# Kernel tuning notes

Measured on AMD Instinct MI355X. Metric: run time of the kernel, lower is better.

The kernel has to match this reference:

```python
import jax, jax.numpy as jnp
import numpy as np

B, T, N = 32, 24, 512
DIM_IN, DIM_OUT, HID, EMB = 64, 2, 128, 16
NEG_SLOPE = 0.01  # nn.LeakyReLU default


def leaky_relu(x):
    return jnp.where(x >= 0, x, NEG_SLOPE * x)


def setup_inputs() -> dict:
    key = jax.random.key(0)
    ks = jax.random.split(key, 11)
    return {
        "eb": jax.random.normal(ks[0], (B, T, N, DIM_IN), jnp.float32),
        "time_eb": jax.random.normal(ks[1], (B, T, EMB), jnp.float32),
        "node_eb": jax.random.normal(ks[2], (N, EMB), jnp.float32),
        # ln1: Linear(dim_in, hidden) stored as [dim_in, hidden] (x @ W + b)
        "W1": jax.random.normal(ks[3], (DIM_IN, HID), jnp.float32) / np.sqrt(DIM_IN),
        "b1": jax.random.normal(ks[4], (HID,), jnp.float32) * 0.01,
        # ln3: Linear(hidden, dim_out)
        "W3": jax.random.normal(ks[5], (HID, DIM_OUT), jnp.float32) / np.sqrt(HID),
        "b3": jax.random.normal(ks[6], (DIM_OUT,), jnp.float32) * 0.01,
        "weights_pool_spa": jax.random.normal(ks[7], (EMB, HID, HID), jnp.float32),
        "bias_pool_spa": jax.random.normal(ks[8], (EMB, HID), jnp.float32),
        "weights_pool_tem": jax.random.normal(ks[9], (EMB, HID, HID), jnp.float32),
        "bias_pool_tem": jax.random.normal(ks[10], (EMB, HID), jnp.float32),
    }


def reference(eb, time_eb, node_eb, W1, b1, W3, b3,
              weights_pool_spa, bias_pool_spa,
              weights_pool_tem, bias_pool_tem):
    # eb: [b,t,n,dim_in] -> [b,t,n,hidden]
    eb_out = eb @ W1 + b1
    # spatial hypernetwork: per-node weight [n,hid,hid] and bias [n,hid]
    weights_spa = jnp.einsum('nd,dio->nio', node_eb, weights_pool_spa)
    bias_spa = node_eb @ bias_pool_spa  # [n,hid]
    out_spa = leaky_relu(jnp.einsum('btni,nio->btno', eb_out, weights_spa) + bias_spa)
    # temporal hypernetwork: per-(b,t) weight [b,t,hid,hid] and bias [b,t,1,hid]
    weights_tem = jnp.einsum('btd,dio->btio', time_eb, weights_pool_tem)
    bias_tem = (time_eb @ bias_pool_tem)[:, :, None, :]
    out_tem = leaky_relu(jnp.einsum('btni,btio->btno', out_spa, weights_tem) + bias_tem)
    logits = out_tem @ W3 + b3  # [b,t,n,dim_out]
    return logits
```

## Files before the change

kernel.cpp:

```cpp
#include <hip/hip_runtime.h>
#include <hip/hip_bf16.h>
#include <stdint.h>

#define BT   768
#define NN   512
#define DIN  64
#define HID  128
#define EMB  16
#define SLOPE 0.01f

typedef __attribute__((ext_vector_type(8))) short bf16x8;
typedef __attribute__((ext_vector_type(4))) float f32x4;
typedef __attribute__((ext_vector_type(4))) short short4v;

__device__ __forceinline__ short f2bf(float f) {
    uint32_t u = __float_as_uint(f);
    u += 0x7fff + ((u >> 16) & 1);
    return (short)(u >> 16);
}
__device__ __forceinline__ float bf2f(short s) {
    return __uint_as_float(((uint32_t)(unsigned short)s) << 16);
}

static const size_t OFF_WSPA = 0;
static const size_t OFF_WTEM = 16777216;
static const size_t OFF_BSPA = 41943040;
static const size_t OFF_BTEM = 42205184;
static const size_t OFF_PTS  = 42598400;
static const size_t OFF_PTT  = 43122688;
static const size_t OFF_W1T  = 43646976;
static const size_t OFF_H2   = 43663360;

__global__ __launch_bounds__(256)
void k_prep(const float* __restrict__ pool_spa, const float* __restrict__ pool_tem,
            const float* __restrict__ W1, short* __restrict__ pts,
            short* __restrict__ ptt, short* __restrict__ w1t)
{
    const int b = blockIdx.x, t = threadIdx.x;
    if (b == 128) {
        int o = t >> 1, kh = (t & 1) * 32;
        for (int k = 0; k < 32; ++k)
            w1t[o * 64 + kh + k] = f2bf(W1[(kh + k) * HID + o]);
        return;
    }
    const float* pool = (b < 64) ? pool_spa : pool_tem;
    short* outp = (b < 64) ? pts : ptt;
    const int bb = b & 63;
    const int d = bb >> 2, o0 = (bb & 3) * 32;
    __shared__ short s[32 * 136];
    #pragma unroll
    for (int c = 0; c < 16; ++c) {
        int e = c * 256 + t;
        int i = e >> 5, oo = e & 31;
        s[oo * 136 + i] = f2bf(pool[(d * HID + i) * HID + o0 + oo]);
    }
    __syncthreads();
    #pragma unroll
    for (int c = 0; c < 8; ++c) {
        int e = c * 256 + t;
        int oo = e >> 6, ii = (e & 63) * 2;
        uint32_t lo = (unsigned short)s[oo * 136 + ii];
        uint32_t hi = (unsigned short)s[oo * 136 + ii + 1];
        ((uint32_t*)outp)[((d * HID + o0 + oo) * HID + ii) >> 1] = lo | (hi << 16);
    }
}

__global__ __launch_bounds__(256)
void k_genw(const short* __restrict__ pts, const short* __restrict__ ptt,
            const float* __restrict__ node_eb, const float* __restrict__ time_eb,
            short* __restrict__ wspa, short* __restrict__ wtem)
{
    const int t = threadIdx.x;
    const bool spa = blockIdx.y < 8;
    const int nb = spa ? blockIdx.y : blockIdx.y - 8;
    const short* pool = spa ? pts : ptt;
    const float* emb = spa ? node_eb : time_eb;
    short* outp = spa ? wspa : wtem;
    __shared__ float sEmb[64 * EMB];
    #pragma unroll
    for (int c = 0; c < 4; ++c) {
        int idx = c * 256 + t;
        sEmb[idx] = emb[nb * 64 * EMB + idx];
    }
    __syncthreads();
    const int cq = blockIdx.x * 256 + t;
    float4 p[EMB];
    #pragma unroll
    for (int d = 0; d < EMB; ++d) {
        short4v v = ((const short4v*)pool)[d * 4096 + cq];
        p[d] = make_float4(bf2f(v.x), bf2f(v.y), bf2f(v.z), bf2f(v.w));
    }
    for (int nn = 0; nn < 64; ++nn) {
        float4 a = make_float4(0.f, 0.f, 0.f, 0.f);
        #pragma unroll
        for (int d = 0; d < EMB; ++d) {
            float e = sEmb[nn * EMB + d];
            a.x += e * p[d].x; a.y += e * p[d].y;
            a.z += e * p[d].z; a.w += e * p[d].w;
        }
        short4v o;
        o.x = f2bf(a.x); o.y = f2bf(a.y); o.z = f2bf(a.z); o.w = f2bf(a.w);
        ((short4v*)outp)[(size_t)(nb * 64 + nn) * 4096 + cq] = o;
    }
}

__global__ __launch_bounds__(256)
void k_genb(const float* __restrict__ bp_spa, const float* __restrict__ bp_tem,
            const float* __restrict__ node_eb, const float* __restrict__ time_eb,
            float* __restrict__ bspa, float* __restrict__ btem)
{
    int q = blockIdx.x * 256 + threadIdx.x;
    const float *bp, *emb; float* outp;
    if (q < NN * 32) { bp = bp_spa; emb = node_eb; outp = bspa; }
    else { q -= NN * 32; bp = bp_tem; emb = time_eb; outp = btem; }
    const int n = q >> 5, oq = q & 31;
    float4 a = make_float4(0.f, 0.f, 0.f, 0.f);
    #pragma unroll
    for (int d = 0; d < EMB; ++d) {
        float e = emb[n * EMB + d];
        float4 b = ((const float4*)bp)[d * 32 + oq];
        a.x += e * b.x; a.y += e * b.y; a.z += e * b.z; a.w += e * b.w;
    }
    ((float4*)outp)[q] = a;
}

__global__ __launch_bounds__(256)
void k_spatial(const float* __restrict__ eb, const short* __restrict__ w1t,
               const float* __restrict__ b1, const short* __restrict__ wspa,
               const float* __restrict__ bspa, short* __restrict__ h2)
{
    const int n = blockIdx.x, R0 = blockIdx.y * 64;
    const int t = threadIdx.x;
    const int wave = t >> 6, lane = t & 63, quad = lane >> 4, l15 = lane & 15;
    const int m0 = (wave >> 1) * 32, n0 = (wave & 1) * 64;

    __shared__ short sH1[64 * 136];
    __shared__ short sU[128 * 136];
    __shared__ float sB1[128], sBs[128];
    short* sEb = sU;
    short* sW1 = sU + 64 * 72;
    short* sWs = sU;

    #pragma unroll
    for (int c = 0; c < 4; ++c) {
        int idx = c * 256 + t;
        int r = idx >> 4, kq = (idx & 15) * 4;
        float4 v = *(const float4*)(eb + ((size_t)(R0 + r) * NN + n) * DIN + kq);
        short4v s;
        s.x = f2bf(v.x); s.y = f2bf(v.y); s.z = f2bf(v.z); s.w = f2bf(v.w);
        *(short4v*)(sEb + r * 72 + kq) = s;
    }
    #pragma unroll
    for (int c = 0; c < 4; ++c) {
        int idx = c * 256 + t;
        *(bf16x8*)(sW1 + (idx >> 3) * 72 + (idx & 7) * 8) =
            *(const bf16x8*)(w1t + idx * 8);
    }
    if (t < 128) { sB1[t] = b1[t]; sBs[t] = bspa[n * HID + t]; }
    __syncthreads();

    f32x4 acc1[2][4] = {};
    #pragma unroll
    for (int kc = 0; kc < 2; ++kc) {
        bf16x8 a0 = *(const bf16x8*)(sEb + (m0 + l15) * 72 + kc * 32 + quad * 8);
        bf16x8 a1 = *(const bf16x8*)(sEb + (m0 + 16 + l15) * 72 + kc * 32 + quad * 8);
        #pragma unroll
        for (int tc = 0; tc < 4; ++tc) {
            bf16x8 b = *(const bf16x8*)(sW1 + (n0 + tc * 16 + l15) * 72 + kc * 32 + quad * 8);
            acc1[0][tc] = __builtin_amdgcn_mfma_f32_16x16x32_bf16(a0, b, acc1[0][tc], 0, 0, 0);
            acc1[1][tc] = __builtin_amdgcn_mfma_f32_16x16x32_bf16(a1, b, acc1[1][tc], 0, 0, 0);
        }
    }
    #pragma unroll
    for (int tr = 0; tr < 2; ++tr)
        #pragma unroll
        for (int tc = 0; tc < 4; ++tc) {
            int col = n0 + tc * 16 + l15;
            float bb = sB1[col];
            #pragma unroll
            for (int r = 0; r < 4; ++r)
                sH1[(m0 + tr * 16 + quad * 4 + r) * 136 + col] = f2bf(acc1[tr][tc][r] + bb);
        }
    __syncthreads();

    {
        const bf16x8* src = (const bf16x8*)(wspa + (size_t)n * 16384);
        #pragma unroll
        for (int c = 0; c < 8; ++c) {
            int idx = c * 256 + t;
            *(bf16x8*)(sWs + (idx >> 4) * 136 + (idx & 15) * 8) = src[idx];
        }
    }
    __syncthreads();

    f32x4 acc2[2][4] = {};
    #pragma unroll
    for (int kc = 0; kc < 4; ++kc) {
        bf16x8 a0 = *(const bf16x8*)(sH1 + (m0 + l15) * 136 + kc * 32 + quad * 8);
        bf16x8 a1 = *(const bf16x8*)(sH1 + (m0 + 16 + l15) * 136 + kc * 32 + quad * 8);
        #pragma unroll
        for (int tc = 0; tc < 4; ++tc) {
            bf16x8 b = *(const bf16x8*)(sWs + (n0 + tc * 16 + l15) * 136 + kc * 32 + quad * 8);
            acc2[0][tc] = __builtin_amdgcn_mfma_f32_16x16x32_bf16(a0, b, acc2[0][tc], 0, 0, 0);
            acc2[1][tc] = __builtin_amdgcn_mfma_f32_16x16x32_bf16(a1, b, acc2[1][tc], 0, 0, 0);
        }
    }
    __syncthreads();
    #pragma unroll
    for (int tr = 0; tr < 2; ++tr)
        #pragma unroll
        for (int tc = 0; tc < 4; ++tc) {
            int col = n0 + tc * 16 + l15;
            float bb = sBs[col];
            #pragma unroll
            for (int r = 0; r < 4; ++r) {
                float v = acc2[tr][tc][r] + bb;
                v = (v >= 0.f) ? v : SLOPE * v;
                sH1[(m0 + tr * 16 + quad * 4 + r) * 136 + col] = f2bf(v);
            }
        }
    __syncthreads();
    #pragma unroll
    for (int c = 0; c < 4; ++c) {
        int idx = c * 256 + t;
        int row = idx >> 4, col = (idx & 15) * 8;
        *(bf16x8*)(h2 + ((size_t)(R0 + row) * NN + n) * HID + col) =
            *(const bf16x8*)(sH1 + row * 136 + col);
    }
}

__global__ __launch_bounds__(256)
void k_temporal(const short* __restrict__ h2, const short* __restrict__ wtem,
                const float* __restrict__ btem, const float* __restrict__ W3,
                const float* __restrict__ b3, float* __restrict__ out)
{
    const int R = blockIdx.x, t = threadIdx.x;
    const int wave = t >> 6, lane = t & 63, quad = lane >> 4, l15 = lane & 15;
    const int m0 = wave * 16;

    __shared__ short sWt[128 * 136];
    __shared__ short sH2[64 * 136];
    __shared__ float sBt[128], sW3[256];

    {
        const bf16x8* src = (const bf16x8*)(wtem + (size_t)R * 16384);
        #pragma unroll
        for (int c = 0; c < 8; ++c) {
            int idx = c * 256 + t;
            *(bf16x8*)(sWt + (idx >> 4) * 136 + (idx & 15) * 8) = src[idx];
        }
    }
    if (t < 128) sBt[t] = btem[R * HID + t];
    sW3[t] = W3[t];
    const float b30 = b3[0], b31 = b3[1];

    for (int nt = 0; nt < 8; ++nt) {
        __syncthreads();
        const bf16x8* src = (const bf16x8*)(h2 + ((size_t)R * NN + nt * 64) * HID);
        #pragma unroll
        for (int c = 0; c < 4; ++c) {
            int idx = c * 256 + t;
            *(bf16x8*)(sH2 + (idx >> 4) * 136 + (idx & 15) * 8) = src[idx];
        }
        __syncthreads();

        f32x4 acc[8] = {};
        #pragma unroll
        for (int kc = 0; kc < 4; ++kc) {
            bf16x8 a = *(const bf16x8*)(sH2 + (m0 + l15) * 136 + kc * 32 + quad * 8);
            #pragma unroll
            for (int tc = 0; tc < 8; ++tc) {
                bf16x8 b = *(const bf16x8*)(sWt + (tc * 16 + l15) * 136 + kc * 32 + quad * 8);
                acc[tc] = __builtin_amdgcn_mfma_f32_16x16x32_bf16(a, b, acc[tc], 0, 0, 0);
            }
        }
        float pl[4][2] = {};
        #pragma unroll
        for (int tc = 0; tc < 8; ++tc) {
            int o = tc * 16 + l15;
            float bt = sBt[o], w0 = sW3[2 * o], w1 = sW3[2 * o + 1];
            #pragma unroll
            for (int r = 0; r < 4; ++r) {
                float v = acc[tc][r] + bt;
                v = (v >= 0.f) ? v : SLOPE * v;
                pl[r][0] += v * w0;
                pl[r][1] += v * w1;
            }
        }
        #pragma unroll
        for (int m = 1; m <= 8; m <<= 1)
            #pragma unroll
            for (int r = 0; r < 4; ++r) {
                pl[r][0] += __shfl_xor(pl[r][0], m);
                pl[r][1] += __shfl_xor(pl[r][1], m);
            }
        if (l15 == 0) {
            #pragma unroll
            for (int r = 0; r < 4; ++r) {
                int nrow = nt * 64 + m0 + quad * 4 + r;
                *(float2*)(out + ((size_t)R * NN + nrow) * 2) =
                    make_float2(pl[r][0] + b30, pl[r][1] + b31);
            }
        }
    }
}

extern "C" void kernel_launch(void* const* d_in, const int* in_sizes, int n_in,
                              void* d_out, int out_size, void* d_ws, size_t ws_size,
                              hipStream_t stream) {
    const float* eb        = (const float*)d_in[0];
    const float* time_eb   = (const float*)d_in[1];
    const float* node_eb   = (const float*)d_in[2];
    const float* W1        = (const float*)d_in[3];
    const float* b1        = (const float*)d_in[4];
    const float* W3        = (const float*)d_in[5];
    const float* b3        = (const float*)d_in[6];
    const float* pool_spa  = (const float*)d_in[7];
    const float* bpool_spa = (const float*)d_in[8];
    const float* pool_tem  = (const float*)d_in[9];
    const float* bpool_tem = (const float*)d_in[10];
    float* out = (float*)d_out;

    char* ws = (char*)d_ws;
    short* wspa = (short*)(ws + OFF_WSPA);
    short* wtem = (short*)(ws + OFF_WTEM);
    float* bspa = (float*)(ws + OFF_BSPA);
    float* btem = (float*)(ws + OFF_BTEM);
    short* pts  = (short*)(ws + OFF_PTS);
    short* ptt  = (short*)(ws + OFF_PTT);
    short* w1t  = (short*)(ws + OFF_W1T);
    short* h2   = (short*)(ws + OFF_H2);

    k_prep<<<129, 256, 0, stream>>>(pool_spa, pool_tem, W1, pts, ptt, w1t);
    k_genw<<<dim3(16, 20), 256, 0, stream>>>(pts, ptt, node_eb, time_eb, wspa, wtem);
    k_genb<<<160, 256, 0, stream>>>(bpool_spa, bpool_tem, node_eb, time_eb, bspa, btem);
    k_spatial<<<dim3(NN, 12), 256, 0, stream>>>(eb, w1t, b1, wspa, bspa, h2);
    k_temporal<<<BT, 256, 0, stream>>>(h2, wtem, btem, W3, b3, out);
}
```

Before: 248.3 us.

## Fuse bias generation into prep, register-prefetch loads, split temporal kernel over nodes

Folds the k_genb bias-generation work into k_prep as extra blocks, removing one kernel launch. k_spatial now issues all of its global loads (eb, W1, per-node weights, biases) up front into registers so their latency overlaps, and keeps the biases in registers instead of shared memory. k_temporal is split into two blocks per (b,t) over the node dimension, which doubles the grid, and it prefetches the next h2 tile into registers while the current tile is computed. The cost is higher register pressure and the per-(b,t) temporal weight tile now being loaded twice.

```diff
diff --git a/kernel.cpp b/kernel.cpp
--- a/kernel.cpp
+++ b/kernel.cpp
@@ -33,10 +33,30 @@
 
 __global__ __launch_bounds__(256)
 void k_prep(const float* __restrict__ pool_spa, const float* __restrict__ pool_tem,
-            const float* __restrict__ W1, short* __restrict__ pts,
-            short* __restrict__ ptt, short* __restrict__ w1t)
+            const float* __restrict__ W1,
+            const float* __restrict__ bp_spa, const float* __restrict__ bp_tem,
+            const float* __restrict__ node_eb, const float* __restrict__ time_eb,
+            short* __restrict__ pts, short* __restrict__ ptt,
+            short* __restrict__ w1t, float* __restrict__ bspa,
+            float* __restrict__ btem)
 {
     const int b = blockIdx.x, t = threadIdx.x;
+    if (b >= 129) {
+        int q = (b - 129) * 256 + t;
+        const float *bp, *emb; float* outp;
+        if (q < NN * 32) { bp = bp_spa; emb = node_eb; outp = bspa; }
+        else { q -= NN * 32; bp = bp_tem; emb = time_eb; outp = btem; }
+        const int n = q >> 5, oq = q & 31;
+        float4 a = make_float4(0.f, 0.f, 0.f, 0.f);
+        #pragma unroll
+        for (int d = 0; d < EMB; ++d) {
+            float e = emb[n * EMB + d];
+            float4 bv = ((const float4*)bp)[d * 32 + oq];
+            a.x += e * bv.x; a.y += e * bv.y; a.z += e * bv.z; a.w += e * bv.w;
+        }
+        ((float4*)outp)[q] = a;
+        return;
+    }
     if (b == 128) {
         int o = t >> 1, kh = (t & 1) * 32;
         for (int k = 0; k < 32; ++k)
@@ -105,26 +125,6 @@
 }
 
 __global__ __launch_bounds__(256)
-void k_genb(const float* __restrict__ bp_spa, const float* __restrict__ bp_tem,
-            const float* __restrict__ node_eb, const float* __restrict__ time_eb,
-            float* __restrict__ bspa, float* __restrict__ btem)
-{
-    int q = blockIdx.x * 256 + threadIdx.x;
-    const float *bp, *emb; float* outp;
-    if (q < NN * 32) { bp = bp_spa; emb = node_eb; outp = bspa; }
-    else { q -= NN * 32; bp = bp_tem; emb = time_eb; outp = btem; }
-    const int n = q >> 5, oq = q & 31;
-    float4 a = make_float4(0.f, 0.f, 0.f, 0.f);
-    #pragma unroll
-    for (int d = 0; d < EMB; ++d) {
-        float e = emb[n * EMB + d];
-        float4 b = ((const float4*)bp)[d * 32 + oq];
-        a.x += e * b.x; a.y += e * b.y; a.z += e * b.z; a.w += e * b.w;
-    }
-    ((float4*)outp)[q] = a;
-}
-
-__global__ __launch_bounds__(256)
 void k_spatial(const float* __restrict__ eb, const short* __restrict__ w1t,
                const float* __restrict__ b1, const short* __restrict__ wspa,
                const float* __restrict__ bspa, short* __restrict__ h2)
@@ -136,27 +136,47 @@
 
     __shared__ short sH1[64 * 136];
     __shared__ short sU[128 * 136];
-    __shared__ float sB1[128], sBs[128];
     short* sEb = sU;
     short* sW1 = sU + 64 * 72;
     short* sWs = sU;
 
+    float4 ev[4];
     #pragma unroll
     for (int c = 0; c < 4; ++c) {
         int idx = c * 256 + t;
         int r = idx >> 4, kq = (idx & 15) * 4;
-        float4 v = *(const float4*)(eb + ((size_t)(R0 + r) * NN + n) * DIN + kq);
+        ev[c] = *(const float4*)(eb + ((size_t)(R0 + r) * NN + n) * DIN + kq);
+    }
+    bf16x8 w1v[4];
+    #pragma unroll
+    for (int c = 0; c < 4; ++c) w1v[c] = ((const bf16x8*)w1t)[c * 256 + t];
+    float b1r[4], bsr[4];
+    #pragma unroll
+    for (int tc = 0; tc < 4; ++tc) {
+        int col = n0 + tc * 16 + l15;
+        b1r[tc] = b1[col];
+        bsr[tc] = bspa[n * HID + col];
+    }
+    bf16x8 wreg[8];
+    {
+        const bf16x8* src = (const bf16x8*)(wspa + (size_t)n * 16384);
+        #pragma unroll
+        for (int c = 0; c < 8; ++c) wreg[c] = src[c * 256 + t];
+    }
+    #pragma unroll
+    for (int c = 0; c < 4; ++c) {
+        int idx = c * 256 + t;
+        int r = idx >> 4, kq = (idx & 15) * 4;
         short4v s;
-        s.x = f2bf(v.x); s.y = f2bf(v.y); s.z = f2bf(v.z); s.w = f2bf(v.w);
+        s.x = f2bf(ev[c].x); s.y = f2bf(ev[c].y);
+        s.z = f2bf(ev[c].z); s.w = f2bf(ev[c].w);
         *(short4v*)(sEb + r * 72 + kq) = s;
     }
     #pragma unroll
     for (int c = 0; c < 4; ++c) {
         int idx = c * 256 + t;
-        *(bf16x8*)(sW1 + (idx >> 3) * 72 + (idx & 7) * 8) =
-            *(const bf16x8*)(w1t + idx * 8);
-    }
-    if (t < 128) { sB1[t] = b1[t]; sBs[t] = bspa[n * HID + t]; }
+        *(bf16x8*)(sW1 + (idx >> 3) * 72 + (idx & 7) * 8) = w1v[c];
+    }
     __syncthreads();
 
     f32x4 acc1[2][4] = {};
@@ -176,20 +196,16 @@
         #pragma unroll
         for (int tc = 0; tc < 4; ++tc) {
             int col = n0 + tc * 16 + l15;
-            float bb = sB1[col];
             #pragma unroll
             for (int r = 0; r < 4; ++r)
-                sH1[(m0 + tr * 16 + quad * 4 + r) * 136 + col] = f2bf(acc1[tr][tc][r] + bb);
-        }
-    __syncthreads();
-
-    {
-        const bf16x8* src = (const bf16x8*)(wspa + (size_t)n * 16384);
-        #pragma unroll
-        for (int c = 0; c < 8; ++c) {
-            int idx = c * 256 + t;
-            *(bf16x8*)(sWs + (idx >> 4) * 136 + (idx & 15) * 8) = src[idx];
-        }
+                sH1[(m0 + tr * 16 + quad * 4 + r) * 136 + col] = f2bf(acc1[tr][tc][r] + b1r[tc]);
+        }
+    __syncthreads();
+
+    #pragma unroll
+    for (int c = 0; c < 8; ++c) {
+        int idx = c * 256 + t;
+        *(bf16x8*)(sWs + (idx >> 4) * 136 + (idx & 15) * 8) = wreg[c];
     }
     __syncthreads();
 
@@ -211,10 +227,9 @@
         #pragma unroll
         for (int tc = 0; tc < 4; ++tc) {
             int col = n0 + tc * 16 + l15;
-            float bb = sBs[col];
             #pragma unroll
             for (int r = 0; r < 4; ++r) {
-                float v = acc2[tr][tc][r] + bb;
+                float v = acc2[tr][tc][r] + bsr[tc];
                 v = (v >= 0.f) ? v : SLOPE * v;
                 sH1[(m0 + tr * 16 + quad * 4 + r) * 136 + col] = f2bf(v);
             }
@@ -234,36 +249,53 @@
                 const float* __restrict__ btem, const float* __restrict__ W3,
                 const float* __restrict__ b3, float* __restrict__ out)
 {
-    const int R = blockIdx.x, t = threadIdx.x;
+    const int R = blockIdx.x, nbase = blockIdx.y * 256;
+    const int t = threadIdx.x;
     const int wave = t >> 6, lane = t & 63, quad = lane >> 4, l15 = lane & 15;
     const int m0 = wave * 16;
 
     __shared__ short sWt[128 * 136];
     __shared__ short sH2[64 * 136];
-    __shared__ float sBt[128], sW3[256];
-
+
+    bf16x8 wv[8];
     {
         const bf16x8* src = (const bf16x8*)(wtem + (size_t)R * 16384);
         #pragma unroll
-        for (int c = 0; c < 8; ++c) {
-            int idx = c * 256 + t;
-            *(bf16x8*)(sWt + (idx >> 4) * 136 + (idx & 15) * 8) = src[idx];
-        }
-    }
-    if (t < 128) sBt[t] = btem[R * HID + t];
-    sW3[t] = W3[t];
+        for (int c = 0; c < 8; ++c) wv[c] = src[c * 256 + t];
+    }
+    bf16x8 hreg[4];
+    {
+        const bf16x8* src = (const bf16x8*)(h2 + ((size_t)R * NN + nbase) * HID);
+        #pragma unroll
+        for (int c = 0; c < 4; ++c) hreg[c] = src[c * 256 + t];
+    }
+    float btr[8], w3r0[8], w3r1[8];
+    #pragma unroll
+    for (int tc = 0; tc < 8; ++tc) {
+        int o = tc * 16 + l15;
+        btr[tc] = btem[R * HID + o];
+        w3r0[tc] = W3[2 * o]; w3r1[tc] = W3[2 * o + 1];
+    }
     const float b30 = b3[0], b31 = b3[1];
 
-    for (int nt = 0; nt < 8; ++nt) {
-        __syncthreads();
-        const bf16x8* src = (const bf16x8*)(h2 + ((size_t)R * NN + nt * 64) * HID);
-        #pragma unroll
-        for (int c = 0; c < 4; ++c) {
-            int idx = c * 256 + t;
-            *(bf16x8*)(sH2 + (idx >> 4) * 136 + (idx & 15) * 8) = src[idx];
-        }
-        __syncthreads();
-
+    #pragma unroll
+    for (int c = 0; c < 8; ++c) {
+        int idx = c * 256 + t;
+        *(bf16x8*)(sWt + (idx >> 4) * 136 + (idx & 15) * 8) = wv[c];
+    }
+    #pragma unroll
+    for (int c = 0; c < 4; ++c) {
+        int idx = c * 256 + t;
+        *(bf16x8*)(sH2 + (idx >> 4) * 136 + (idx & 15) * 8) = hreg[c];
+    }
+    __syncthreads();
+
+    for (int nt = 0; nt < 4; ++nt) {
+        if (nt < 3) {
+            const bf16x8* src = (const bf16x8*)(h2 + ((size_t)R * NN + nbase + (nt + 1) * 64) * HID);
+            #pragma unroll
+            for (int c = 0; c < 4; ++c) hreg[c] = src[c * 256 + t];
+        }
         f32x4 acc[8] = {};
         #pragma unroll
         for (int kc = 0; kc < 4; ++kc) {
@@ -277,14 +309,12 @@
         float pl[4][2] = {};
         #pragma unroll
         for (int tc = 0; tc < 8; ++tc) {
-            int o = tc * 16 + l15;
-            float bt = sBt[o], w0 = sW3[2 * o], w1 = sW3[2 * o + 1];
             #pragma unroll
             for (int r = 0; r < 4; ++r) {
-                float v = acc[tc][r] + bt;
+                float v = acc[tc][r] + btr[tc];
                 v = (v >= 0.f) ? v : SLOPE * v;
-                pl[r][0] += v * w0;
-                pl[r][1] += v * w1;
+                pl[r][0] += v * w3r0[tc];
+                pl[r][1] += v * w3r1[tc];
             }
         }
         #pragma unroll
@@ -297,10 +327,19 @@
         if (l15 == 0) {
             #pragma unroll
             for (int r = 0; r < 4; ++r) {
-                int nrow = nt * 64 + m0 + quad * 4 + r;
+                int nrow = nbase + nt * 64 + m0 + quad * 4 + r;
                 *(float2*)(out + ((size_t)R * NN + nrow) * 2) =
                     make_float2(pl[r][0] + b30, pl[r][1] + b31);
             }
+        }
+        __syncthreads();
+        if (nt < 3) {
+            #pragma unroll
+            for (int c = 0; c < 4; ++c) {
+                int idx = c * 256 + t;
+                *(bf16x8*)(sH2 + (idx >> 4) * 136 + (idx & 15) * 8) = hreg[c];
+            }
+            __syncthreads();
         }
     }
 }
@@ -331,9 +370,9 @@
     short* w1t  = (short*)(ws + OFF_W1T);
     short* h2   = (short*)(ws + OFF_H2);
 
-    k_prep<<<129, 256, 0, stream>>>(pool_spa, pool_tem, W1, pts, ptt, w1t);
+    k_prep<<<289, 256, 0, stream>>>(pool_spa, pool_tem, W1, bpool_spa, bpool_tem,
+                                    node_eb, time_eb, pts, ptt, w1t, bspa, btem);
     k_genw<<<dim3(16, 20), 256, 0, stream>>>(pts, ptt, node_eb, time_eb, wspa, wtem);
-    k_genb<<<160, 256, 0, stream>>>(bpool_spa, bpool_tem, node_eb, time_eb, bspa, btem);
     k_spatial<<<dim3(NN, 12), 256, 0, stream>>>(eb, w1t, b1, wspa, bspa, h2);
-    k_temporal<<<BT, 256, 0, stream>>>(h2, wtem, btem, W3, b3, out);
-}
+    k_temporal<<<dim3(BT, 2), 256, 0, stream>>>(h2, wtem, btem, W3, b3, out);
+}
```

After: 244.8 us. Within noise of the previous version (-1.4%).
